# Performance work log

Measured on AMD Instinct MI355X. Metric: run time of the kernel, lower is better.

Reference implementation:

```python
import jax, jax.numpy as jnp
import numpy as np

BETA = 0.1
EPS_LOW = 0.2
EPS_HIGH = 0.2
TEMPERATURE = 1.0


def setup_inputs() -> dict:
    key = jax.random.key(0)
    ks = jax.random.split(key, 6)
    B, T, H, V = 4, 1024, 2048, 32000
    x = jax.random.normal(ks[0], (B, T, H), dtype=jnp.float32)
    ref_input = jax.random.normal(ks[1], (B, T, H), dtype=jnp.float32)
    W = jax.random.normal(ks[2], (V, H), dtype=jnp.float32) * (1.0 / np.sqrt(H))
    ref_W = jax.random.normal(ks[3], (V, H), dtype=jnp.float32) * (1.0 / np.sqrt(H))
    selected_token_ids = jax.random.randint(ks[4], (B, T), 0, V, dtype=jnp.int64)
    attention_mask = jnp.ones((B, T), dtype=jnp.float32)
    advantages = jax.random.normal(ks[5], (B,), dtype=jnp.float32)
    return {
        "x": x,
        "W": W,
        "ref_W": ref_W,
        "ref_input": ref_input,
        "selected_token_ids": selected_token_ids,
        "attention_mask": attention_mask,
        "advantages": advantages,
    }


def _per_token_logps_and_mean(h, W, ids):
    # h: [B,T,H], W: [V,H] -> logits [B,T,V]
    logits = jnp.einsum("bth,vh->btv", h, W)
    if TEMPERATURE != 1.0:
        logits = logits / TEMPERATURE
    log_probs = jax.nn.log_softmax(logits, axis=-1)
    ptl = jnp.take_along_axis(log_probs, ids[..., None], axis=-1)[..., 0]
    return ptl, log_probs.mean()


def reference(x, W, ref_W, ref_input, selected_token_ids, attention_mask, advantages):
    per_token_logps, log_probs_mean = _per_token_logps_and_mean(x, W, selected_token_ids)

    # reference model path (no grad)
    ref_per_token_logps, _ = _per_token_logps_and_mean(
        jax.lax.stop_gradient(ref_input), jax.lax.stop_gradient(ref_W), selected_token_ids
    )
    ref_per_token_logps = jax.lax.stop_gradient(ref_per_token_logps)

    old_per_token_logps = jax.lax.stop_gradient(per_token_logps)
    coef_1 = jnp.exp(per_token_logps - old_per_token_logps)
    coef_2 = jnp.clip(coef_1, 1.0 - EPS_LOW, 1.0 + EPS_HIGH)
    adv = advantages[:, None]  # [B,1]
    per_token_loss = -jnp.minimum(coef_1 * adv, coef_2 * adv)

    delta = ref_per_token_logps - per_token_logps
    kl_div = jnp.exp(delta) - delta - 1.0
    per_token_loss = per_token_loss + BETA * kl_div

    loss = (per_token_loss * attention_mask).sum() / jnp.clip(attention_mask.sum(), 1.0)

    kl_metric = ((kl_div * attention_mask).sum(axis=1) / jnp.clip(attention_mask.sum(axis=1), 1.0)).mean()
    return loss, per_token_logps.mean(), log_probs_mean, kl_metric
```

## Files before the change

### kernel.cpp

```cpp
#include <hip/hip_runtime.h>
#include <stdint.h>

#define M_TOK 4096
#define N_VOC 32000
#define K_DIM 2048
#define BM 256
#define BN 256
#define BK 64
#define NT (K_DIM / BK)
#define BETA 0.1f
#define W_SCALE 32.0f
#define INV_W_SCALE (1.0f / 32.0f)

typedef float f32x4 __attribute__((ext_vector_type(4)));

__global__ __launch_bounds__(256) void cast_f32_fp8(const float* __restrict__ in,
                                                    unsigned* __restrict__ out, int n4,
                                                    float scale) {
  int i = blockIdx.x * blockDim.x + threadIdx.x;
  int stride = gridDim.x * blockDim.x;
  const float4* __restrict__ in4 = (const float4*)in;
  for (; i < n4; i += stride) {
    float4 f = in4[i];
    int v = __builtin_amdgcn_cvt_pk_fp8_f32(f.x * scale, f.y * scale, 0, false);
    v = __builtin_amdgcn_cvt_pk_fp8_f32(f.z * scale, f.w * scale, v, true);
    out[i] = (unsigned)v;
  }
}

__global__ __launch_bounds__(512, 2) void gemm_stats(
    const unsigned char* __restrict__ A,
    const unsigned char* __restrict__ B,
    const int* __restrict__ ids,
    float* __restrict__ S, float* __restrict__ L, float* __restrict__ sel) {
  __shared__ unsigned char lds[65536];

  const int tid = threadIdx.x;
  const int w = tid >> 6;
  const int l = tid & 63;
  const int m0 = blockIdx.y * BM;
  const int n0 = blockIdx.x * BN;
  const int wm = w >> 2, wn = w & 3;
  const int l15 = l & 15, quad = l >> 4;

  const int srow = l >> 2;
  const int sc = (l & 3) ^ (srow & 3) ^ ((srow >> 2) & 3);
  const size_t sOff = (size_t)srow * K_DIM + (size_t)(sc * 16);
  const unsigned char* pA = A + (size_t)(m0 + w * 32) * K_DIM + sOff;
  const unsigned char* pB = B + (size_t)(n0 + w * 32) * K_DIM + sOff;
  const size_t RS16 = (size_t)16 * K_DIM;

  unsigned char* dA = &lds[w * 2048];
  unsigned char* dB = &lds[16384 + w * 2048];

  const int sw = (l15 & 3) ^ ((l15 >> 2) & 3);
  const int roff = l15 * 64 + (((quad >> 1) ^ sw) << 4) + (quad & 1) * 8;

  f32x4 acc[8][4];
  const f32x4 zero = {0.f, 0.f, 0.f, 0.f};
#pragma unroll
  for (int i = 0; i < 8; ++i)
#pragma unroll
    for (int j = 0; j < 4; ++j) acc[i][j] = zero;

#define GLL(src, dst)                                                              \
  __builtin_amdgcn_global_load_lds(                                                \
      (const __attribute__((address_space(1))) unsigned int*)(src),                \
      (__attribute__((address_space(3))) unsigned int*)(dst), 16, 0, 0)

#define STAGE_A(nb, kn)                                                            \
  do {                                                                            \
    GLL(pA + (kn), dA + (nb)*32768);                                              \
    GLL(pA + (kn) + RS16, dA + (nb)*32768 + 1024);                                \
  } while (0)

#define STAGE_B(nb, kn)                                                            \
  do {                                                                            \
    GLL(pB + (kn), dB + (nb)*32768);                                              \
    GLL(pB + (kn) + RS16, dB + (nb)*32768 + 1024);                                \
  } while (0)

#define PHASE(bf, p)                                                               \
  do {                                                                            \
    const unsigned char* Abase = &lds[(bf)*32768 + wm*8192];                       \
    const unsigned char* Bbase = &lds[(bf)*32768 + 16384 + wn*4096];               \
    const int ro = roff ^ ((p) << 5);                                              \
    long long af[8], bq[4];                                                        \
    _Pragma("unroll") for (int i = 0; i < 8; ++i)                                  \
        af[i] = *(const long long*)(Abase + i * 1024 + ro);                        \
    _Pragma("unroll") for (int j = 0; j < 4; ++j)                                  \
        bq[j] = *(const long long*)(Bbase + j * 1024 + ro);                        \
    __builtin_amdgcn_s_setprio(1);                                                 \
    _Pragma("unroll") for (int i = 0; i < 8; ++i)                                  \
      _Pragma("unroll") for (int j = 0; j < 4; ++j)                                \
        acc[i][j] = __builtin_amdgcn_mfma_f32_16x16x32_fp8_fp8(af[i], bq[j],       \
                                                               acc[i][j], 0, 0, 0);\
    __builtin_amdgcn_s_setprio(0);                                                 \
  } while (0)

  STAGE_A(0, 0);
  STAGE_B(0, 0);

  for (int t = 0; t < NT - 1; ++t) {
    const int bf = t & 1, nb = bf ^ 1;
    const int kn = (t + 1) * BK;
    asm volatile("s_waitcnt vmcnt(0)" ::: "memory");
    __builtin_amdgcn_s_barrier();
    asm volatile("" ::: "memory");
    STAGE_A(nb, kn);
    PHASE(bf, 0);
    STAGE_B(nb, kn);
    PHASE(bf, 1);
  }
  asm volatile("s_waitcnt vmcnt(0)" ::: "memory");
  __builtin_amdgcn_s_barrier();
  asm volatile("" ::: "memory");
  PHASE(1, 0);
  PHASE(1, 1);

#undef GLL
#undef STAGE_A
#undef STAGE_B
#undef PHASE

#pragma unroll
  for (int i = 0; i < 8; ++i) {
#pragma unroll
    for (int r = 0; r < 4; ++r) {
      int row = m0 + wm * 128 + i * 16 + quad * 4 + r;
      int sid = ids[row];
      int loc = sid - n0 - wn * 64;
      bool hit = (loc >= 0) && (loc < 64) && ((loc & 15) == l15);
      float es = 0.f, ls = 0.f, selv = 0.f;
#pragma unroll
      for (int j = 0; j < 4; ++j) {
        float v = acc[i][j][r] * INV_W_SCALE;
        es += __expf(v);
        ls += v;
        if (hit && ((loc >> 4) == j)) selv = v;
      }
      if (hit) sel[row] = selv;
#pragma unroll
      for (int mk = 1; mk < 16; mk <<= 1) {
        es += __shfl_xor(es, mk);
        ls += __shfl_xor(ls, mk);
      }
      if (l15 == 0) {
        atomicAdd(&S[row], es);
        atomicAdd(&L[row], ls);
      }
    }
  }
}

__global__ __launch_bounds__(1024) void finalize_kernel(
    const float* __restrict__ S1, const float* __restrict__ L1, const float* __restrict__ P1,
    const float* __restrict__ S2, const float* __restrict__ P2,
    const float* __restrict__ mask, const float* __restrict__ adv, float* __restrict__ out) {
  __shared__ float red[12];
  int tid = threadIdx.x;
  int lane = tid & 63;
  if (tid < 12) red[tid] = 0.f;
  __syncthreads();

  float loss_num = 0.f, mask_sum = 0.f, ptl_sum = 0.f, lpm_sum = 0.f;
  float klb[4] = {0.f, 0.f, 0.f, 0.f}, mb[4] = {0.f, 0.f, 0.f, 0.f};
#pragma unroll
  for (int k = 0; k < 4; ++k) {
    int t = k * 1024 + tid;
    float lse1 = logf(S1[t]);
    float ptl = P1[t] - lse1;
    float ref_ptl = P2[t] - logf(S2[t]);
    float d = ref_ptl - ptl;
    float kl = expf(d) - d - 1.f;
    float m = mask[t];
    float a = adv[k];
    loss_num += (-a + BETA * kl) * m;
    mask_sum += m;
    ptl_sum += ptl;
    lpm_sum += L1[t] * (1.f / (float)N_VOC) - lse1;
    klb[k] += kl * m;
    mb[k] += m;
  }
  float vals[12] = {loss_num, mask_sum, ptl_sum, lpm_sum,
                    klb[0], klb[1], klb[2], klb[3],
                    mb[0],  mb[1],  mb[2],  mb[3]};
#pragma unroll
  for (int v = 0; v < 12; ++v) {
    float xv = vals[v];
#pragma unroll
    for (int mk = 32; mk >= 1; mk >>= 1) xv += __shfl_xor(xv, mk);
    if (lane == 0) atomicAdd(&red[v], xv);
  }
  __syncthreads();
  if (tid == 0) {
    float loss = red[0] / fmaxf(red[1], 1.f);
    float km = 0.f;
#pragma unroll
    for (int b = 0; b < 4; ++b) km += red[4 + b] / fmaxf(red[8 + b], 1.f);
    out[0] = loss;
    out[1] = red[2] * (1.f / 4096.f);
    out[2] = red[3] * (1.f / 4096.f);
    out[3] = km * 0.25f;
  }
}

extern "C" void kernel_launch(void* const* d_in, const int* in_sizes, int n_in,
                              void* d_out, int out_size, void* d_ws, size_t ws_size,
                              hipStream_t stream) {
  const float* x = (const float*)d_in[0];
  const float* W = (const float*)d_in[1];
  const float* ref_W = (const float*)d_in[2];
  const float* ref_x = (const float*)d_in[3];
  const int* ids = (const int*)d_in[4];
  const float* mask = (const float*)d_in[5];
  const float* adv = (const float*)d_in[6];
  float* out = (float*)d_out;

  char* ws = (char*)d_ws;
  unsigned char* Wq = (unsigned char*)ws;
  unsigned char* xq = (unsigned char*)(ws + (size_t)N_VOC * K_DIM);
  float* accum = (float*)(ws + (size_t)N_VOC * K_DIM + (size_t)M_TOK * K_DIM);
  float* S1 = accum;
  float* L1 = accum + 4096;
  float* P1 = accum + 8192;
  float* S2 = accum + 12288;
  float* L2 = accum + 16384;
  float* P2 = accum + 20480;

  hipMemsetAsync(accum, 0, 6 * 4096 * sizeof(float), stream);

  dim3 grid(N_VOC / BN, M_TOK / BM);

  cast_f32_fp8<<<2048, 256, 0, stream>>>(W, (unsigned*)Wq, N_VOC * K_DIM / 4, W_SCALE);
  cast_f32_fp8<<<512, 256, 0, stream>>>(x, (unsigned*)xq, M_TOK * K_DIM / 4, 1.0f);
  gemm_stats<<<grid, 512, 0, stream>>>(xq, Wq, ids, S1, L1, P1);

  cast_f32_fp8<<<2048, 256, 0, stream>>>(ref_W, (unsigned*)Wq, N_VOC * K_DIM / 4, W_SCALE);
  cast_f32_fp8<<<512, 256, 0, stream>>>(ref_x, (unsigned*)xq, M_TOK * K_DIM / 4, 1.0f);
  gemm_stats<<<grid, 512, 0, stream>>>(xq, Wq, ids, S2, L2, P2);

  finalize_kernel<<<1, 1024, 0, stream>>>(S1, L1, P1, S2, P2, mask, adv, out);
}
```

Before: 1.745 ms.

## Triple-buffer LDS with interleaved quarter-tile loads and barrier-fenced MFMA phases

Moves the fp8 GEMM main loop from double to triple LDS buffering (96KB), prefetching two K-tiles ahead and waiting with vmcnt(4) so one tile's loads stay in flight. Each tile is split into four sub-phases that interleave half-tile global->LDS loads with 16-MFMA groups, separated by barriers and sched_barriers in a ping-pong style. The aim is to hide global load latency and spread LDS reads between MFMA bursts. The cost is more LDS per block, which may cut occupancy from 2 blocks/CU, plus many extra barriers.

```diff
diff --git a/kernel.cpp b/kernel.cpp
--- a/kernel.cpp
+++ b/kernel.cpp
@@ -33,7 +33,7 @@
     const unsigned char* __restrict__ B,
     const int* __restrict__ ids,
     float* __restrict__ S, float* __restrict__ L, float* __restrict__ sel) {
-  __shared__ unsigned char lds[65536];
+  __shared__ unsigned char lds[3 * 32768];
 
   const int tid = threadIdx.x;
   const int w = tid >> 6;
@@ -45,16 +45,16 @@
 
   const int srow = l >> 2;
   const int sc = (l & 3) ^ (srow & 3) ^ ((srow >> 2) & 3);
-  const size_t sOff = (size_t)srow * K_DIM + (size_t)(sc * 16);
-  const unsigned char* pA = A + (size_t)(m0 + w * 32) * K_DIM + sOff;
-  const unsigned char* pB = B + (size_t)(n0 + w * 32) * K_DIM + sOff;
-  const size_t RS16 = (size_t)16 * K_DIM;
-
-  unsigned char* dA = &lds[w * 2048];
-  unsigned char* dB = &lds[16384 + w * 2048];
+  const unsigned char* pA = A + (size_t)(m0 + w * 16 + srow) * K_DIM + sc * 16;
+  const unsigned char* pB = B + (size_t)(n0 + w * 16 + srow) * K_DIM + sc * 16;
+  const size_t HS = (size_t)128 * K_DIM;
+
+  unsigned char* dA = &lds[w * 1024];
+  unsigned char* dB = &lds[16384 + w * 1024];
 
   const int sw = (l15 & 3) ^ ((l15 >> 2) & 3);
-  const int roff = l15 * 64 + (((quad >> 1) ^ sw) << 4) + (quad & 1) * 8;
+  const int aoffBase = wm * 8192 + l15 * 64 + (((quad >> 1) ^ sw) << 4) + (quad & 1) * 8;
+  const int boffBase = 16384 + wn * 4096 + l15 * 64 + (((quad >> 1) ^ sw) << 4) + (quad & 1) * 8;
 
   f32x4 acc[8][4];
   const f32x4 zero = {0.f, 0.f, 0.f, 0.f};
@@ -68,60 +68,76 @@
       (const __attribute__((address_space(1))) unsigned int*)(src),                \
       (__attribute__((address_space(3))) unsigned int*)(dst), 16, 0, 0)
 
-#define STAGE_A(nb, kn)                                                            \
-  do {                                                                            \
-    GLL(pA + (kn), dA + (nb)*32768);                                              \
-    GLL(pA + (kn) + RS16, dA + (nb)*32768 + 1024);                                \
-  } while (0)
-
-#define STAGE_B(nb, kn)                                                            \
-  do {                                                                            \
-    GLL(pB + (kn), dB + (nb)*32768);                                              \
-    GLL(pB + (kn) + RS16, dB + (nb)*32768 + 1024);                                \
-  } while (0)
-
-#define PHASE(bf, p)                                                               \
-  do {                                                                            \
-    const unsigned char* Abase = &lds[(bf)*32768 + wm*8192];                       \
-    const unsigned char* Bbase = &lds[(bf)*32768 + 16384 + wn*4096];               \
-    const int ro = roff ^ ((p) << 5);                                              \
-    long long af[8], bq[4];                                                        \
-    _Pragma("unroll") for (int i = 0; i < 8; ++i)                                  \
-        af[i] = *(const long long*)(Abase + i * 1024 + ro);                        \
-    _Pragma("unroll") for (int j = 0; j < 4; ++j)                                  \
-        bq[j] = *(const long long*)(Bbase + j * 1024 + ro);                        \
+#define STAGE_A_H(b, h, kn) GLL(pA + HS * (h) + (kn), dA + (b) * 32768 + (h) * 8192)
+#define STAGE_B_H(b, h, kn) GLL(pB + HS * (h) + (kn), dB + (b) * 32768 + (h) * 8192)
+
+#define LOAD_B(rd, ks)                                                             \
+  _Pragma("unroll") for (int j = 0; j < 4; ++j)                                    \
+      bq[j] = *(const long long*)(&lds[(rd) * 32768] +                             \
+                                  ((boffBase ^ ((ks) << 5)) + j * 1024));
+
+#define LOAD_A(rd, ks, ih)                                                         \
+  _Pragma("unroll") for (int i = 0; i < 4; ++i)                                    \
+      af[i] = *(const long long*)(&lds[(rd) * 32768] +                             \
+                                  ((aoffBase ^ ((ks) << 5)) + ((ih) * 4 + i) * 1024));
+
+#define MFMA16(ih)                                                                 \
+  do {                                                                             \
     __builtin_amdgcn_s_setprio(1);                                                 \
-    _Pragma("unroll") for (int i = 0; i < 8; ++i)                                  \
+    _Pragma("unroll") for (int i = 0; i < 4; ++i)                                  \
       _Pragma("unroll") for (int j = 0; j < 4; ++j)                                \
-        acc[i][j] = __builtin_amdgcn_mfma_f32_16x16x32_fp8_fp8(af[i], bq[j],       \
-                                                               acc[i][j], 0, 0, 0);\
+        acc[(ih) * 4 + i][j] = __builtin_amdgcn_mfma_f32_16x16x32_fp8_fp8(         \
+            af[i], bq[j], acc[(ih) * 4 + i][j], 0, 0, 0);                          \
     __builtin_amdgcn_s_setprio(0);                                                 \
   } while (0)
 
-  STAGE_A(0, 0);
-  STAGE_B(0, 0);
-
-  for (int t = 0; t < NT - 1; ++t) {
-    const int bf = t & 1, nb = bf ^ 1;
-    const int kn = (t + 1) * BK;
-    asm volatile("s_waitcnt vmcnt(0)" ::: "memory");
-    __builtin_amdgcn_s_barrier();
-    asm volatile("" ::: "memory");
-    STAGE_A(nb, kn);
-    PHASE(bf, 0);
-    STAGE_B(nb, kn);
-    PHASE(bf, 1);
-  }
-  asm volatile("s_waitcnt vmcnt(0)" ::: "memory");
-  __builtin_amdgcn_s_barrier();
-  asm volatile("" ::: "memory");
-  PHASE(1, 0);
-  PHASE(1, 1);
+#define PRE_MFMA_BAR()                                                             \
+  do {                                                                             \
+    __builtin_amdgcn_s_barrier();                                                  \
+    __builtin_amdgcn_sched_barrier(0);                                             \
+  } while (0)
+
+#define TILE_CORE(rd, S0, S1, S2, S3, VWAIT)                                       \
+  do {                                                                             \
+    asm volatile("s_waitcnt vmcnt(" VWAIT ")" ::: "memory");                       \
+    __builtin_amdgcn_s_barrier();                                                  \
+    long long af[4], bq[4];                                                        \
+    LOAD_B(rd, 0); LOAD_A(rd, 0, 0); S0;                                           \
+    PRE_MFMA_BAR(); MFMA16(0); __builtin_amdgcn_s_barrier();                       \
+    LOAD_A(rd, 0, 1); S1;                                                          \
+    PRE_MFMA_BAR(); MFMA16(1); __builtin_amdgcn_s_barrier();                       \
+    LOAD_B(rd, 1); LOAD_A(rd, 1, 0); S2;                                           \
+    PRE_MFMA_BAR(); MFMA16(0); __builtin_amdgcn_s_barrier();                       \
+    LOAD_A(rd, 1, 1); S3;                                                          \
+    PRE_MFMA_BAR(); MFMA16(1); __builtin_amdgcn_s_barrier();                       \
+  } while (0)
+
+#define TILE_S(rd, w2, kn2)                                                        \
+  TILE_CORE(rd, STAGE_A_H(w2, 0, kn2), STAGE_B_H(w2, 0, kn2),                      \
+            STAGE_A_H(w2, 1, kn2), STAGE_B_H(w2, 1, kn2), "4")
+#define TILE_N(rd, VW) TILE_CORE(rd, (void)0, (void)0, (void)0, (void)0, VW)
+
+  STAGE_A_H(0, 0, 0); STAGE_B_H(0, 0, 0); STAGE_A_H(0, 1, 0); STAGE_B_H(0, 1, 0);
+  STAGE_A_H(1, 0, BK); STAGE_B_H(1, 0, BK); STAGE_A_H(1, 1, BK); STAGE_B_H(1, 1, BK);
+
+  for (int tb = 0; tb < NT - 2; tb += 3) {
+    TILE_S(0, 2, (tb + 2) * BK);
+    TILE_S(1, 0, (tb + 3) * BK);
+    TILE_S(2, 1, (tb + 4) * BK);
+  }
+  TILE_N(0, "4");
+  TILE_N(1, "0");
 
 #undef GLL
-#undef STAGE_A
-#undef STAGE_B
-#undef PHASE
+#undef STAGE_A_H
+#undef STAGE_B_H
+#undef LOAD_A
+#undef LOAD_B
+#undef MFMA16
+#undef PRE_MFMA_BAR
+#undef TILE_CORE
+#undef TILE_S
+#undef TILE_N
 
 #pragma unroll
   for (int i = 0; i < 8; ++i) {
```

After: 1.784 ms. +2.2%, slower.
